# Kernel tuning notes

Measured on AMD Instinct MI355X. Metric: run time of the kernel, lower is better.

The kernel has to match this reference:

```python
import jax, jax.numpy as jnp
import numpy as np

B, N, DM, H = 32, 256, 512, 8
DH = DM // H  # 64, also dim_g of the geometric embedding


def setup_inputs() -> dict:
    key = jax.random.key(0)
    ks = jax.random.split(key, 16)
    s = 0.02
    inp = {
        "v": jax.random.normal(ks[0], (B, N, DM), jnp.float32),
        "k": jax.random.normal(ks[1], (B, N, DM), jnp.float32),
        "q": jax.random.normal(ks[2], (B, N, DM), jnp.float32),
        "box": jax.random.uniform(ks[3], (B, N, 4), jnp.float32),
        "mask": jax.random.randint(ks[4], (B, 1, 1, N), 0, 2).astype(bool),
        "fg": 2,
        "Wq": jax.random.normal(ks[5], (DM, DM), jnp.float32) * s,
        "bq": jnp.zeros((DM,), jnp.float32),
        "Wk": jax.random.normal(ks[6], (DM, DM), jnp.float32) * s,
        "bk": jnp.zeros((DM,), jnp.float32),
        "Wv": jax.random.normal(ks[7], (DM, DM), jnp.float32) * s,
        "bv": jnp.zeros((DM,), jnp.float32),
        "Wm": jax.random.normal(ks[8], (DM, DM), jnp.float32) * s,
        "bm": jnp.zeros((DM,), jnp.float32),
        "Wbox": jax.random.normal(ks[9], (DH, 1), jnp.float32) * s,
        "bbox": jnp.zeros((1,), jnp.float32),
    }
    return inp


def positional_embedding(box, dim_g, wave_len=1000.0):
    # box: [B, N, 4] -> embedding [B, N, N, dim_g]
    x_min, y_min, x_max, y_max = jnp.split(box, 4, axis=-1)  # each [B, N, 1]
    cx = (x_min + x_max) * 0.5
    cy = (y_min + y_max) * 0.5
    w = x_max - x_min + 1.0
    h = y_max - y_min + 1.0
    # pairwise deltas [B, N, N]
    dx = jnp.log(jnp.maximum(jnp.abs((cx - jnp.swapaxes(cx, -2, -1)) / w), 1e-3))
    dy = jnp.log(jnp.maximum(jnp.abs((cy - jnp.swapaxes(cy, -2, -1)) / h), 1e-3))
    dw = jnp.log(w / jnp.swapaxes(w, -2, -1))
    dh = jnp.log(h / jnp.swapaxes(h, -2, -1))
    pos = jnp.stack([dx, dy, dw, dh], axis=-1)  # [B, N, N, 4]
    n_freq = dim_g // 8
    feat_range = jnp.arange(n_freq, dtype=jnp.float32)
    dim_mat = 1.0 / (wave_len ** (feat_range / float(n_freq)))  # [n_freq]
    mul = (100.0 * pos)[..., None] * dim_mat  # [B, N, N, 4, n_freq]
    mul = mul.reshape(pos.shape[0], pos.shape[1], pos.shape[2], -1)  # [B,N,N,dim_g/2]
    return jnp.concatenate([jnp.sin(mul), jnp.cos(mul)], axis=-1)  # [B,N,N,dim_g]


def reference(v, k, q, box, mask, fg, Wq, bq, Wk, bk, Wv, bv, Wm, bm, Wbox, bbox):
    # fg == 2 branch: geometric box positional bias (pos_scores computed here)
    nb = q.shape[0]

    def heads(x, W, b):
        return (x @ W + b).reshape(nb, -1, H, DH).transpose(0, 2, 1, 3)  # [B,H,N,Dh]

    qh, kh, vh = heads(q, Wq, bq), heads(k, Wk, bk), heads(v, Wv, bv)
    scale = 1.0 / jnp.sqrt(jnp.float32(DH))
    scores = jnp.einsum('bhqd,bhkd->bhqk', qh, kh) * scale  # [B,H,N,N]

    # original loops over heads recomputing the identical embedding/linear;
    # compute once and tile across heads (same math)
    emb = positional_embedding(box, DH)                 # [B,N,N,DH]
    ps = jax.nn.relu(emb @ Wbox + bbox)[..., 0]          # [B,N,N]
    pos_scores = jnp.tile(ps[:, None], (1, H, 1, 1))     # [B,H,N,N]

    scores = scores + pos_scores
    scores = jnp.where(mask, jnp.float32(-1e9), scores)
    att = jax.nn.softmax(scores, axis=-1)  # dropout is identity at inference
    out = jnp.einsum('bhqk,bhkd->bhqd', att, vh)
    out = out.transpose(0, 2, 1, 3).reshape(nb, -1, DM)
    atted = out @ Wm + bm
    return atted, pos_scores
```

## Files before the change

### kernel.cpp

```cpp
#include <hip/hip_runtime.h>


typedef __bf16 bf16_t;
typedef __bf16 bf16x8 __attribute__((ext_vector_type(8)));
typedef float  f32x4  __attribute__((ext_vector_type(4)));
typedef float  f32x8  __attribute__((ext_vector_type(8)));

#define NB    32
#define NSEQ  256
#define DMODEL 512
#define NH    8
#define DHEAD 64
#define M_ROWS (NB * NSEQ)
#define ATTED_ELEMS (M_ROWS * DMODEL)
#define HEAD_T_ELEMS 4194304

#define WS_WT    0
#define WS_QH    1048576
#define WS_ATTW  13631488

__device__ inline bf16x8 load8(const bf16_t* p) { return *(const bf16x8*)p; }
__device__ inline bf16x8 load8(const float* p) {
  f32x8 v = *(const f32x8*)p;
  bf16x8 r;
#pragma unroll
  for (int j = 0; j < 8; j++) r[j] = (bf16_t)v[j];
  return r;
}

__global__ __launch_bounds__(256) void transpose_kernel(
    const float* __restrict__ W0, const float* __restrict__ W1,
    const float* __restrict__ W2, const float* __restrict__ W3,
    bf16_t* __restrict__ wt) {
  __shared__ float T_s[64 * 65];
  int tid = threadIdx.x;
  int m = blockIdx.z;
  const float* W = (m == 0) ? W0 : (m == 1) ? W1 : (m == 2) ? W2 : W3;
  bf16_t* WT = wt + m * (DMODEL * DMODEL);
  int k0 = blockIdx.x * 64, n0 = blockIdx.y * 64;
#pragma unroll
  for (int i = 0; i < 16; i++) {
    int idx = tid + i * 256;
    int r = idx >> 6, c = idx & 63;
    T_s[r * 65 + c] = W[(size_t)(k0 + r) * DMODEL + n0 + c];
  }
  __syncthreads();
#pragma unroll
  for (int i = 0; i < 16; i++) {
    int idx = tid + i * 256;
    int r = idx >> 6, c = idx & 63;
    WT[(size_t)(n0 + r) * DMODEL + k0 + c] = (bf16_t)T_s[c * 65 + r];
  }
}

__global__ __launch_bounds__(256) void pos_kernel(
    const float* __restrict__ box, const float* __restrict__ Wbox,
    const float* __restrict__ bbox, float* __restrict__ pos_out) {
  __shared__ float wb[64];
  __shared__ float bb;
  int tid = threadIdx.x;
  if (tid < 64) wb[tid] = Wbox[tid];
  if (tid == 0) bb = bbox[0];
  __syncthreads();

  int bx = blockIdx.x;
  int b = bx >> 8, i = bx & 255, j = tid;

  float4 bi = *(const float4*)(box + (size_t)(b * NSEQ + i) * 4);
  float4 bj = *(const float4*)(box + (size_t)(b * NSEQ + j) * 4);

  float cxi = (bi.x + bi.z) * 0.5f, cyi = (bi.y + bi.w) * 0.5f;
  float wi = bi.z - bi.x + 1.0f,    hi = bi.w - bi.y + 1.0f;
  float cxj = (bj.x + bj.z) * 0.5f, cyj = (bj.y + bj.w) * 0.5f;
  float wj = bj.z - bj.x + 1.0f,    hj = bj.w - bj.y + 1.0f;

  float dx = __logf(fmaxf(fabsf((cxi - cxj) / wi), 1e-3f));
  float dy = __logf(fmaxf(fabsf((cyi - cyj) / hi), 1e-3f));
  float dw = __logf(wi / wj);
  float dh = __logf(hi / hj);

  const float dim_mat[8] = {1.0f, 0.42169650342f, 0.177827941f, 0.074989421f,
                            0.0316227766f, 0.0133352143f, 0.00562341325f, 0.00237137371f};
  float p4[4] = {dx, dy, dw, dh};
  float acc = bb;
#pragma unroll
  for (int c = 0; c < 4; c++) {
    float base = 100.0f * p4[c];
#pragma unroll
    for (int f = 0; f < 8; f++) {
      float sn, cs;
      __sincosf(base * dim_mat[f], &sn, &cs);
      acc += sn * wb[c * 8 + f] + cs * wb[32 + c * 8 + f];
    }
  }
  float pv = fmaxf(acc, 0.0f);
  size_t base_bi = ((size_t)b * NH * NSEQ + i) * NSEQ + j;
#pragma unroll
  for (int h = 0; h < NH; h++)
    pos_out[base_bi + (size_t)h * NSEQ * NSEQ] = pv;
}

template <typename AT>
__global__ __launch_bounds__(256) void gemm128_kernel(
    const AT* __restrict__ A0, const AT* __restrict__ A1, const AT* __restrict__ A2,
    const bf16_t* __restrict__ WTbase,
    const float* __restrict__ bias0, const float* __restrict__ bias1,
    const float* __restrict__ bias2,
    bf16_t* __restrict__ outb,
    float* __restrict__ outf,
    int final_mode) {
  __shared__ bf16_t A_s[128 * 40];
  __shared__ bf16_t B_s[128 * 40];

  int tid = threadIdx.x;
  int wave = tid >> 6, lane = tid & 63, quad = lane >> 4, l16 = lane & 15;
  int wm = wave >> 1, wn = wave & 1;
  int bm = blockIdx.x, bn = blockIdx.y, z = blockIdx.z;

  const AT* A = (z == 0) ? A0 : (z == 1) ? A1 : A2;
  const float* bias = (z == 0) ? bias0 : (z == 1) ? bias1 : bias2;
  const bf16_t* WT = WTbase + (size_t)(final_mode == 2 ? 3 : z) * 262144;
  int mode = (final_mode == 2) ? 2 : ((z == 2) ? 1 : 0);

  f32x4 acc[4][4];
#pragma unroll
  for (int i = 0; i < 4; i++)
#pragma unroll
    for (int j = 0; j < 4; j++) acc[i][j] = (f32x4){0.f, 0.f, 0.f, 0.f};

  for (int kk = 0; kk < 16; kk++) {
    int k0 = kk * 32;
#pragma unroll
    for (int i = 0; i < 2; i++) {
      int flat = tid + i * 256;
      int row = flat >> 2, seg = flat & 3;
      bf16x8 av = load8(A + (size_t)(bm * 128 + row) * DMODEL + k0 + seg * 8);
      *(bf16x8*)(A_s + row * 40 + seg * 8) = av;
      bf16x8 bv = *(const bf16x8*)(WT + (size_t)(bn * 128 + row) * DMODEL + k0 + seg * 8);
      *(bf16x8*)(B_s + row * 40 + seg * 8) = bv;
    }
    __syncthreads();

    bf16x8 a[4], b[4];
#pragma unroll
    for (int i = 0; i < 4; i++)
      a[i] = *(const bf16x8*)(A_s + (wm * 64 + i * 16 + l16) * 40 + quad * 8);
#pragma unroll
    for (int j = 0; j < 4; j++)
      b[j] = *(const bf16x8*)(B_s + (wn * 64 + j * 16 + l16) * 40 + quad * 8);
#pragma unroll
    for (int i = 0; i < 4; i++)
#pragma unroll
      for (int j = 0; j < 4; j++)
        acc[i][j] = __builtin_amdgcn_mfma_f32_16x16x32_bf16(a[i], b[j], acc[i][j], 0, 0, 0);
    __syncthreads();
  }

#pragma unroll
  for (int j = 0; j < 4; j++) {
    int gc = bn * 128 + wn * 64 + j * 16 + l16;
    float bs = bias[gc];
#pragma unroll
    for (int i = 0; i < 4; i++) {
#pragma unroll
      for (int r = 0; r < 4; r++) {
        int gm = bm * 128 + wm * 64 + i * 16 + quad * 4 + r;
        float val = acc[i][j][r] + bs;
        if (mode == 2) {
          outf[(size_t)gm * DMODEL + gc] = val;
        } else {
          int b = gm >> 8, n = gm & 255, h = gc >> 6, d = gc & 63;
          size_t idx = (mode == 0)
              ? ((size_t)(b * NH + h) * NSEQ + n) * DHEAD + d
              : ((size_t)(b * NH + h) * DHEAD + d) * NSEQ + n;
          outb[(size_t)z * HEAD_T_ELEMS + idx] = (bf16_t)val;
        }
      }
    }
  }
}

__global__ __launch_bounds__(256) void attn_kernel(
    const bf16_t* __restrict__ qh, const bf16_t* __restrict__ kh,
    const bf16_t* __restrict__ vT, const float* __restrict__ pos,
    const int* __restrict__ mask, bf16_t* __restrict__ attw) {
  __shared__ bf16_t KP_s[256 * 72];

  int tid = threadIdx.x;
  int wave = tid >> 6, lane = tid & 63, quad = lane >> 4, l16 = lane & 15;
  int qt = blockIdx.x, h = blockIdx.y, b = blockIdx.z;

  const bf16_t* qb = qh + (size_t)(b * NH + h) * NSEQ * DHEAD;
  const bf16_t* kb = kh + (size_t)(b * NH + h) * NSEQ * DHEAD;
  const bf16_t* vb = vT + (size_t)(b * NH + h) * DHEAD * NSEQ;
  const float* pb = pos + (size_t)b * NH * NSEQ * NSEQ;
  const int* mrow = mask + b * NSEQ;

#pragma unroll
  for (int i = 0; i < 8; i++) {
    int flat = tid + i * 256;
    int row = flat >> 3, seg = flat & 7;
    *(bf16x8*)(KP_s + row * 72 + seg * 8) =
        *(const bf16x8*)(kb + (size_t)row * DHEAD + seg * 8);
  }
  __syncthreads();

  int m0 = qt * 64 + wave * 16;

  bf16x8 a0 = *(const bf16x8*)(qb + (size_t)(m0 + l16) * DHEAD + quad * 8);
  bf16x8 a1 = *(const bf16x8*)(qb + (size_t)(m0 + l16) * DHEAD + 32 + quad * 8);
  f32x4 s[16];
#pragma unroll
  for (int t = 0; t < 16; t++) s[t] = (f32x4){0.f, 0.f, 0.f, 0.f};
#pragma unroll
  for (int t = 0; t < 16; t++) {
    const bf16_t* krow = KP_s + (t * 16 + l16) * 72;
    bf16x8 b0 = *(const bf16x8*)(krow + quad * 8);
    bf16x8 b1 = *(const bf16x8*)(krow + 32 + quad * 8);
    s[t] = __builtin_amdgcn_mfma_f32_16x16x32_bf16(a0, b0, s[t], 0, 0, 0);
    s[t] = __builtin_amdgcn_mfma_f32_16x16x32_bf16(a1, b1, s[t], 0, 0, 0);
  }

#pragma unroll
  for (int t = 0; t < 16; t++) {
    int gj = t * 16 + l16;
    int mk = mrow[gj];
#pragma unroll
    for (int r = 0; r < 4; r++) {
      int gr = m0 + quad * 4 + r;
      float v = s[t][r] * 0.125f + pb[(size_t)gr * NSEQ + gj];
      s[t][r] = mk ? -1e9f : v;
    }
  }

  float inv[4];
#pragma unroll
  for (int r = 0; r < 4; r++) {
    float m = -1e30f;
#pragma unroll
    for (int t = 0; t < 16; t++) m = fmaxf(m, s[t][r]);
    m = fmaxf(m, __shfl_xor(m, 1));
    m = fmaxf(m, __shfl_xor(m, 2));
    m = fmaxf(m, __shfl_xor(m, 4));
    m = fmaxf(m, __shfl_xor(m, 8));
    float sum = 0.f;
#pragma unroll
    for (int t = 0; t < 16; t++) {
      float e = __expf(s[t][r] - m);
      s[t][r] = e;
      sum += e;
    }
    sum += __shfl_xor(sum, 1);
    sum += __shfl_xor(sum, 2);
    sum += __shfl_xor(sum, 4);
    sum += __shfl_xor(sum, 8);
    inv[r] = 1.0f / sum;
  }

  __syncthreads();

#pragma unroll
  for (int t = 0; t < 16; t++) {
    int gj = t * 16 + l16;
#pragma unroll
    for (int r = 0; r < 4; r++)
      KP_s[(wave * 16 + quad * 4 + r) * 264 + gj] = (bf16_t)(s[t][r] * inv[r]);
  }

  f32x4 o[4];
#pragma unroll
  for (int t2 = 0; t2 < 4; t2++) o[t2] = (f32x4){0.f, 0.f, 0.f, 0.f};
#pragma unroll
  for (int kk = 0; kk < 8; kk++) {
    bf16x8 pa = *(const bf16x8*)(KP_s + (wave * 16 + l16) * 264 + kk * 32 + quad * 8);
#pragma unroll
    for (int t2 = 0; t2 < 4; t2++) {
      bf16x8 vv = *(const bf16x8*)(vb + (size_t)(t2 * 16 + l16) * NSEQ + kk * 32 + quad * 8);
      o[t2] = __builtin_amdgcn_mfma_f32_16x16x32_bf16(pa, vv, o[t2], 0, 0, 0);
    }
  }

#pragma unroll
  for (int t2 = 0; t2 < 4; t2++) {
    int d = t2 * 16 + l16;
#pragma unroll
    for (int r = 0; r < 4; r++) {
      int gr = m0 + quad * 4 + r;
      attw[(size_t)(b * NSEQ + gr) * DMODEL + h * DHEAD + d] = (bf16_t)o[t2][r];
    }
  }
}

extern "C" void kernel_launch(void* const* d_in, const int* in_sizes, int n_in,
                              void* d_out, int out_size, void* d_ws, size_t ws_size,
                              hipStream_t stream) {
  const float* v    = (const float*)d_in[0];
  const float* k    = (const float*)d_in[1];
  const float* q    = (const float*)d_in[2];
  const float* box  = (const float*)d_in[3];
  const int*   mask = (const int*)d_in[4];
  const float* Wq   = (const float*)d_in[6];
  const float* bq   = (const float*)d_in[7];
  const float* Wk   = (const float*)d_in[8];
  const float* bk   = (const float*)d_in[9];
  const float* Wv   = (const float*)d_in[10];
  const float* bv   = (const float*)d_in[11];
  const float* Wm   = (const float*)d_in[12];
  const float* bm   = (const float*)d_in[13];
  const float* Wbox = (const float*)d_in[14];
  const float* bbox = (const float*)d_in[15];

  float* out  = (float*)d_out;
  bf16_t* ws  = (bf16_t*)d_ws;
  bf16_t* WT   = ws + WS_WT;
  bf16_t* qh   = ws + WS_QH;
  bf16_t* khw  = qh + 1 * HEAD_T_ELEMS;
  bf16_t* vTp  = qh + 2 * HEAD_T_ELEMS;
  bf16_t* attw = ws + WS_ATTW;
  float* pos  = out + ATTED_ELEMS;

  transpose_kernel<<<dim3(8, 8, 4), dim3(256), 0, stream>>>(Wq, Wk, Wv, Wm, WT);
  pos_kernel<<<dim3(NB * NSEQ), dim3(256), 0, stream>>>(box, Wbox, bbox, pos);
  gemm128_kernel<float><<<dim3(64, 4, 3), dim3(256), 0, stream>>>(
      q, k, v, WT, bq, bk, bv, qh, out, 0);
  attn_kernel<<<dim3(NSEQ / 64, NH, NB), dim3(256), 0, stream>>>(
      qh, khw, vTp, pos, mask, attw);
  gemm128_kernel<bf16_t><<<dim3(64, 4, 1), dim3(256), 0, stream>>>(
      attw, attw, attw, WT, bm, bm, bm, qh, out, 2);
}
```

Measured before the change: 248.7 us.

## Register-prefetch GEMM tiles with K=64 steps and hoist attention Q/mask loads

The projection GEMM now loads the next K-tile from global memory into registers while MFMAs run on the current shared-memory tile. The K step is doubled to 64, which halves the number of barriers per tile and needs larger shared buffers (stride 72). The attention kernel issues its Q fragment and mask loads before the K staging and barrier so their latency overlaps. In exchange the GEMM uses more registers, which may lower occupancy.

Measured after the change: 254.3 us. +2.2%, slower.

```diff
diff --git a/kernel.cpp b/kernel.cpp
--- a/kernel.cpp
+++ b/kernel.cpp
@@ -19,9 +19,12 @@
 #define WS_QH    1048576
 #define WS_ATTW  13631488
 
-__device__ inline bf16x8 load8(const bf16_t* p) { return *(const bf16x8*)p; }
-__device__ inline bf16x8 load8(const float* p) {
-  f32x8 v = *(const f32x8*)p;
+template <typename T> struct vec8;
+template <> struct vec8<float>  { using type = f32x8; };
+template <> struct vec8<bf16_t> { using type = bf16x8; };
+
+__device__ inline bf16x8 to_bf16(bf16x8 v) { return v; }
+__device__ inline bf16x8 to_bf16(f32x8 v) {
   bf16x8 r;
 #pragma unroll
   for (int j = 0; j < 8; j++) r[j] = (bf16_t)v[j];
@@ -106,11 +109,9 @@
     const bf16_t* __restrict__ WTbase,
     const float* __restrict__ bias0, const float* __restrict__ bias1,
     const float* __restrict__ bias2,
-    bf16_t* __restrict__ outb,
-    float* __restrict__ outf,
-    int final_mode) {
-  __shared__ bf16_t A_s[128 * 40];
-  __shared__ bf16_t B_s[128 * 40];
+    bf16_t* __restrict__ outb, float* __restrict__ outf, int final_mode) {
+  __shared__ bf16_t A_s[128 * 72];
+  __shared__ bf16_t B_s[128 * 72];
 
   int tid = threadIdx.x;
   int wave = tid >> 6, lane = tid & 63, quad = lane >> 4, l16 = lane & 15;
@@ -122,37 +123,59 @@
   const bf16_t* WT = WTbase + (size_t)(final_mode == 2 ? 3 : z) * 262144;
   int mode = (final_mode == 2) ? 2 : ((z == 2) ? 1 : 0);
 
+  int srow[4], sseg[4];
+#pragma unroll
+  for (int i = 0; i < 4; i++) {
+    int flat = tid + i * 256;
+    srow[i] = flat >> 3;
+    sseg[i] = flat & 7;
+  }
+
+  typename vec8<AT>::type areg[4];
+  bf16x8 breg[4];
+
+  auto load_tiles = [&](int k0) {
+#pragma unroll
+    for (int i = 0; i < 4; i++) {
+      areg[i] = *(const typename vec8<AT>::type*)
+          (A + (size_t)(bm * 128 + srow[i]) * DMODEL + k0 + sseg[i] * 8);
+      breg[i] = *(const bf16x8*)
+          (WT + (size_t)(bn * 128 + srow[i]) * DMODEL + k0 + sseg[i] * 8);
+    }
+  };
+
+  load_tiles(0);
+
   f32x4 acc[4][4];
 #pragma unroll
   for (int i = 0; i < 4; i++)
 #pragma unroll
     for (int j = 0; j < 4; j++) acc[i][j] = (f32x4){0.f, 0.f, 0.f, 0.f};
 
-  for (int kk = 0; kk < 16; kk++) {
-    int k0 = kk * 32;
-#pragma unroll
-    for (int i = 0; i < 2; i++) {
-      int flat = tid + i * 256;
-      int row = flat >> 2, seg = flat & 3;
-      bf16x8 av = load8(A + (size_t)(bm * 128 + row) * DMODEL + k0 + seg * 8);
-      *(bf16x8*)(A_s + row * 40 + seg * 8) = av;
-      bf16x8 bv = *(const bf16x8*)(WT + (size_t)(bn * 128 + row) * DMODEL + k0 + seg * 8);
-      *(bf16x8*)(B_s + row * 40 + seg * 8) = bv;
+  for (int kk = 0; kk < 8; kk++) {
+#pragma unroll
+    for (int i = 0; i < 4; i++) {
+      *(bf16x8*)(A_s + srow[i] * 72 + sseg[i] * 8) = to_bf16(areg[i]);
+      *(bf16x8*)(B_s + srow[i] * 72 + sseg[i] * 8) = breg[i];
     }
     __syncthreads();
-
-    bf16x8 a[4], b[4];
-#pragma unroll
-    for (int i = 0; i < 4; i++)
-      a[i] = *(const bf16x8*)(A_s + (wm * 64 + i * 16 + l16) * 40 + quad * 8);
-#pragma unroll
-    for (int j = 0; j < 4; j++)
-      b[j] = *(const bf16x8*)(B_s + (wn * 64 + j * 16 + l16) * 40 + quad * 8);
-#pragma unroll
-    for (int i = 0; i < 4; i++)
+    if (kk < 7) load_tiles((kk + 1) * 64);
+
+#pragma unroll
+    for (int c = 0; c < 2; c++) {
+      bf16x8 a[4], b[4];
+#pragma unroll
+      for (int i = 0; i < 4; i++)
+        a[i] = *(const bf16x8*)(A_s + (wm * 64 + i * 16 + l16) * 72 + c * 32 + quad * 8);
 #pragma unroll
       for (int j = 0; j < 4; j++)
-        acc[i][j] = __builtin_amdgcn_mfma_f32_16x16x32_bf16(a[i], b[j], acc[i][j], 0, 0, 0);
+        b[j] = *(const bf16x8*)(B_s + (wn * 64 + j * 16 + l16) * 72 + c * 32 + quad * 8);
+#pragma unroll
+      for (int i = 0; i < 4; i++)
+#pragma unroll
+        for (int j = 0; j < 4; j++)
+          acc[i][j] = __builtin_amdgcn_mfma_f32_16x16x32_bf16(a[i], b[j], acc[i][j], 0, 0, 0);
+    }
     __syncthreads();
   }
 
@@ -196,6 +219,14 @@
   const float* pb = pos + (size_t)b * NH * NSEQ * NSEQ;
   const int* mrow = mask + b * NSEQ;
 
+  int m0 = qt * 64 + wave * 16;
+
+  bf16x8 a0 = *(const bf16x8*)(qb + (size_t)(m0 + l16) * DHEAD + quad * 8);
+  bf16x8 a1 = *(const bf16x8*)(qb + (size_t)(m0 + l16) * DHEAD + 32 + quad * 8);
+  int mk[16];
+#pragma unroll
+  for (int t = 0; t < 16; t++) mk[t] = mrow[t * 16 + l16];
+
 #pragma unroll
   for (int i = 0; i < 8; i++) {
     int flat = tid + i * 256;
@@ -205,10 +236,6 @@
   }
   __syncthreads();
 
-  int m0 = qt * 64 + wave * 16;
-
-  bf16x8 a0 = *(const bf16x8*)(qb + (size_t)(m0 + l16) * DHEAD + quad * 8);
-  bf16x8 a1 = *(const bf16x8*)(qb + (size_t)(m0 + l16) * DHEAD + 32 + quad * 8);
   f32x4 s[16];
 #pragma unroll
   for (int t = 0; t < 16; t++) s[t] = (f32x4){0.f, 0.f, 0.f, 0.f};
@@ -224,12 +251,11 @@
 #pragma unroll
   for (int t = 0; t < 16; t++) {
     int gj = t * 16 + l16;
-    int mk = mrow[gj];
 #pragma unroll
     for (int r = 0; r < 4; r++) {
       int gr = m0 + quad * 4 + r;
       float v = s[t][r] * 0.125f + pb[(size_t)gr * NSEQ + gj];
-      s[t][r] = mk ? -1e9f : v;
+      s[t][r] = mk[t] ? -1e9f : v;
     }
   }
 
```

## Pre-convert inputs to bf16 and stage GEMM tiles via direct global-to-LDS loads

Applied to the files above, without the earlier changes.

Adds a conversion kernel that casts q/k/v to bf16 into the pos output buffer as scratch, so the QKV projection GEMM reads bf16 instead of fp32. The GEMM is rewritten to use global_load_lds direct-to-shared copies with an unpadded 32-wide tile. The output projection uses half-height tiles for more blocks. Q and K are now stored row-major [B,N,DM] and the attention kernel reads them with a head stride, with mask loads hoisted. This trades an extra pass over the inputs and possible LDS bank conflicts from removing padding for cheaper GEMM loads and simpler stores.

New measurement: 240.3 us. 1.04x faster.

```diff
diff --git a/kernel.cpp b/kernel.cpp
--- a/kernel.cpp
+++ b/kernel.cpp
@@ -2,9 +2,10 @@
 
 
 typedef __bf16 bf16_t;
+typedef __bf16 bf16x4 __attribute__((ext_vector_type(4)));
 typedef __bf16 bf16x8 __attribute__((ext_vector_type(8)));
 typedef float  f32x4  __attribute__((ext_vector_type(4)));
-typedef float  f32x8  __attribute__((ext_vector_type(8)));
+typedef unsigned int u32;
 
 #define NB    32
 #define NSEQ  256
@@ -19,13 +20,22 @@
 #define WS_QH    1048576
 #define WS_ATTW  13631488
 
-__device__ inline bf16x8 load8(const bf16_t* p) { return *(const bf16x8*)p; }
-__device__ inline bf16x8 load8(const float* p) {
-  f32x8 v = *(const f32x8*)p;
-  bf16x8 r;
-#pragma unroll
-  for (int j = 0; j < 8; j++) r[j] = (bf16_t)v[j];
-  return r;
+__device__ inline void glds16(const bf16_t* g, bf16_t* l) {
+  __builtin_amdgcn_global_load_lds(
+      (const __attribute__((address_space(1))) u32*)g,
+      (__attribute__((address_space(3))) u32*)l, 16, 0, 0);
+}
+
+__global__ __launch_bounds__(256) void cvt_kernel(
+    const float* __restrict__ q, const float* __restrict__ k,
+    const float* __restrict__ v, bf16_t* __restrict__ dst) {
+  int z = blockIdx.y;
+  const float* s = (z == 0) ? q : (z == 1) ? k : v;
+  size_t i = ((size_t)blockIdx.x * 256 + threadIdx.x) * 4;
+  float4 x = *(const float4*)(s + i);
+  bf16x4 y;
+  y[0] = (bf16_t)x.x; y[1] = (bf16_t)x.y; y[2] = (bf16_t)x.z; y[3] = (bf16_t)x.w;
+  *(bf16x4*)(dst + (size_t)z * HEAD_T_ELEMS + i) = y;
 }
 
 __global__ __launch_bounds__(256) void transpose_kernel(
@@ -100,56 +110,60 @@
     pos_out[base_bi + (size_t)h * NSEQ * NSEQ] = pv;
 }
 
-template <typename AT>
-__global__ __launch_bounds__(256) void gemm128_kernel(
-    const AT* __restrict__ A0, const AT* __restrict__ A1, const AT* __restrict__ A2,
-    const bf16_t* __restrict__ WTbase,
+template <int IF>
+__global__ __launch_bounds__(256) void gemm_glds(
+    const bf16_t* __restrict__ A0, const bf16_t* __restrict__ A1,
+    const bf16_t* __restrict__ A2, const bf16_t* __restrict__ WTbase,
     const float* __restrict__ bias0, const float* __restrict__ bias1,
     const float* __restrict__ bias2,
-    bf16_t* __restrict__ outb,
-    float* __restrict__ outf,
-    int final_mode) {
-  __shared__ bf16_t A_s[128 * 40];
-  __shared__ bf16_t B_s[128 * 40];
+    bf16_t* __restrict__ outb, float* __restrict__ outf, int final_mode) {
+  constexpr int ROWS = IF * 32;
+  __shared__ bf16_t A_s[ROWS * 32];
+  __shared__ bf16_t B_s[128 * 32];
 
   int tid = threadIdx.x;
   int wave = tid >> 6, lane = tid & 63, quad = lane >> 4, l16 = lane & 15;
   int wm = wave >> 1, wn = wave & 1;
   int bm = blockIdx.x, bn = blockIdx.y, z = blockIdx.z;
 
-  const AT* A = (z == 0) ? A0 : (z == 1) ? A1 : A2;
+  const bf16_t* A = (z == 0) ? A0 : (z == 1) ? A1 : A2;
   const float* bias = (z == 0) ? bias0 : (z == 1) ? bias1 : bias2;
   const bf16_t* WT = WTbase + (size_t)(final_mode == 2 ? 3 : z) * 262144;
   int mode = (final_mode == 2) ? 2 : ((z == 2) ? 1 : 0);
 
-  f32x4 acc[4][4];
-#pragma unroll
-  for (int i = 0; i < 4; i++)
+  int srow = lane >> 2, sseg = (lane & 3) * 8;
+
+  f32x4 acc[IF][4];
+#pragma unroll
+  for (int i = 0; i < IF; i++)
 #pragma unroll
     for (int j = 0; j < 4; j++) acc[i][j] = (f32x4){0.f, 0.f, 0.f, 0.f};
 
   for (int kk = 0; kk < 16; kk++) {
     int k0 = kk * 32;
 #pragma unroll
+    for (int i = 0; i < ROWS / 64; i++) {
+      int r0 = (wave * (ROWS / 64) + i) * 16;
+      glds16(A + (size_t)(bm * ROWS + r0 + srow) * DMODEL + k0 + sseg,
+             A_s + r0 * 32);
+    }
+#pragma unroll
     for (int i = 0; i < 2; i++) {
-      int flat = tid + i * 256;
-      int row = flat >> 2, seg = flat & 3;
-      bf16x8 av = load8(A + (size_t)(bm * 128 + row) * DMODEL + k0 + seg * 8);
-      *(bf16x8*)(A_s + row * 40 + seg * 8) = av;
-      bf16x8 bv = *(const bf16x8*)(WT + (size_t)(bn * 128 + row) * DMODEL + k0 + seg * 8);
-      *(bf16x8*)(B_s + row * 40 + seg * 8) = bv;
+      int r0 = (wave * 2 + i) * 16;
+      glds16(WT + (size_t)(bn * 128 + r0 + srow) * DMODEL + k0 + sseg,
+             B_s + r0 * 32);
     }
     __syncthreads();
 
-    bf16x8 a[4], b[4];
-#pragma unroll
-    for (int i = 0; i < 4; i++)
-      a[i] = *(const bf16x8*)(A_s + (wm * 64 + i * 16 + l16) * 40 + quad * 8);
+    bf16x8 a[IF], b[4];
+#pragma unroll
+    for (int i = 0; i < IF; i++)
+      a[i] = *(const bf16x8*)(A_s + (wm * (IF * 16) + i * 16 + l16) * 32 + quad * 8);
 #pragma unroll
     for (int j = 0; j < 4; j++)
-      b[j] = *(const bf16x8*)(B_s + (wn * 64 + j * 16 + l16) * 40 + quad * 8);
-#pragma unroll
-    for (int i = 0; i < 4; i++)
+      b[j] = *(const bf16x8*)(B_s + (wn * 64 + j * 16 + l16) * 32 + quad * 8);
+#pragma unroll
+    for (int i = 0; i < IF; i++)
 #pragma unroll
       for (int j = 0; j < 4; j++)
         acc[i][j] = __builtin_amdgcn_mfma_f32_16x16x32_bf16(a[i], b[j], acc[i][j], 0, 0, 0);
@@ -161,19 +175,19 @@
     int gc = bn * 128 + wn * 64 + j * 16 + l16;
     float bs = bias[gc];
 #pragma unroll
-    for (int i = 0; i < 4; i++) {
+    for (int i = 0; i < IF; i++) {
 #pragma unroll
       for (int r = 0; r < 4; r++) {
-        int gm = bm * 128 + wm * 64 + i * 16 + quad * 4 + r;
+        int gm = bm * ROWS + wm * (IF * 16) + i * 16 + quad * 4 + r;
         float val = acc[i][j][r] + bs;
         if (mode == 2) {
           outf[(size_t)gm * DMODEL + gc] = val;
+        } else if (mode == 0) {
+          outb[(size_t)z * HEAD_T_ELEMS + (size_t)gm * DMODEL + gc] = (bf16_t)val;
         } else {
           int b = gm >> 8, n = gm & 255, h = gc >> 6, d = gc & 63;
-          size_t idx = (mode == 0)
-              ? ((size_t)(b * NH + h) * NSEQ + n) * DHEAD + d
-              : ((size_t)(b * NH + h) * DHEAD + d) * NSEQ + n;
-          outb[(size_t)z * HEAD_T_ELEMS + idx] = (bf16_t)val;
+          outb[2 * HEAD_T_ELEMS +
+               ((size_t)(b * NH + h) * DHEAD + d) * NSEQ + n] = (bf16_t)val;
         }
       }
     }
@@ -190,25 +204,29 @@
   int wave = tid >> 6, lane = tid & 63, quad = lane >> 4, l16 = lane & 15;
   int qt = blockIdx.x, h = blockIdx.y, b = blockIdx.z;
 
-  const bf16_t* qb = qh + (size_t)(b * NH + h) * NSEQ * DHEAD;
-  const bf16_t* kb = kh + (size_t)(b * NH + h) * NSEQ * DHEAD;
+  const bf16_t* qb = qh + (size_t)(b * NSEQ) * DMODEL + h * DHEAD;
+  const bf16_t* kb = kh + (size_t)(b * NSEQ) * DMODEL + h * DHEAD;
   const bf16_t* vb = vT + (size_t)(b * NH + h) * DHEAD * NSEQ;
   const float* pb = pos + (size_t)b * NH * NSEQ * NSEQ;
   const int* mrow = mask + b * NSEQ;
+
+  int m0 = qt * 64 + wave * 16;
+
+  bf16x8 a0 = *(const bf16x8*)(qb + (size_t)(m0 + l16) * DMODEL + quad * 8);
+  bf16x8 a1 = *(const bf16x8*)(qb + (size_t)(m0 + l16) * DMODEL + 32 + quad * 8);
+  int mk[16];
+#pragma unroll
+  for (int t = 0; t < 16; t++) mk[t] = mrow[t * 16 + l16];
 
 #pragma unroll
   for (int i = 0; i < 8; i++) {
     int flat = tid + i * 256;
     int row = flat >> 3, seg = flat & 7;
     *(bf16x8*)(KP_s + row * 72 + seg * 8) =
-        *(const bf16x8*)(kb + (size_t)row * DHEAD + seg * 8);
+        *(const bf16x8*)(kb + (size_t)row * DMODEL + seg * 8);
   }
   __syncthreads();
 
-  int m0 = qt * 64 + wave * 16;
-
-  bf16x8 a0 = *(const bf16x8*)(qb + (size_t)(m0 + l16) * DHEAD + quad * 8);
-  bf16x8 a1 = *(const bf16x8*)(qb + (size_t)(m0 + l16) * DHEAD + 32 + quad * 8);
   f32x4 s[16];
 #pragma unroll
   for (int t = 0; t < 16; t++) s[t] = (f32x4){0.f, 0.f, 0.f, 0.f};
@@ -224,12 +242,11 @@
 #pragma unroll
   for (int t = 0; t < 16; t++) {
     int gj = t * 16 + l16;
-    int mk = mrow[gj];
 #pragma unroll
     for (int r = 0; r < 4; r++) {
       int gr = m0 + quad * 4 + r;
       float v = s[t][r] * 0.125f + pb[(size_t)gr * NSEQ + gj];
-      s[t][r] = mk ? -1e9f : v;
+      s[t][r] = mk[t] ? -1e9f : v;
     }
   }
 
@@ -318,13 +335,16 @@
   bf16_t* vTp  = qh + 2 * HEAD_T_ELEMS;
   bf16_t* attw = ws + WS_ATTW;
   float* pos  = out + ATTED_ELEMS;
-
+  bf16_t* cvtb = (bf16_t*)pos;
+
+  cvt_kernel<<<dim3(4096, 3), dim3(256), 0, stream>>>(q, k, v, cvtb);
   transpose_kernel<<<dim3(8, 8, 4), dim3(256), 0, stream>>>(Wq, Wk, Wv, Wm, WT);
+  gemm_glds<4><<<dim3(64, 4, 3), dim3(256), 0, stream>>>(
+      cvtb, cvtb + HEAD_T_ELEMS, cvtb + 2 * HEAD_T_ELEMS, WT,
+      bq, bk, bv, qh, out, 0);
   pos_kernel<<<dim3(NB * NSEQ), dim3(256), 0, stream>>>(box, Wbox, bbox, pos);
-  gemm128_kernel<float><<<dim3(64, 4, 3), dim3(256), 0, stream>>>(
-      q, k, v, WT, bq, bk, bv, qh, out, 0);
   attn_kernel<<<dim3(NSEQ / 64, NH, NB), dim3(256), 0, stream>>>(
       qh, khw, vTp, pos, mask, attw);
-  gemm128_kernel<bf16_t><<<dim3(64, 4, 1), dim3(256), 0, stream>>>(
+  gemm_glds<2><<<dim3(128, 4, 1), dim3(256), 0, stream>>>(
       attw, attw, attw, WT, bm, bm, bm, qh, out, 2);
 }
```
